# Performance work log

Hardware: AMD Instinct MI355X
Metric: run time of the kernel (lower is better)

Reference implementation:

```python
import jax, jax.numpy as jnp
import numpy as np

DIM = 128
HEADS = 8
DK = DIM // HEADS
HID = DIM * 4
# torch: scores / math.sqrt(scale) with scale = 1/dim**0.5  ->  multiply by dim**0.25
INV = float(1.0 / np.sqrt(1.0 / np.sqrt(DIM)))


def _ln(x, g, b, eps=1e-5):
    m = jnp.mean(x, axis=-1, keepdims=True)
    v = jnp.mean((x - m) ** 2, axis=-1, keepdims=True)
    return (x - m) / jnp.sqrt(v + eps) * g + b


def _lin(x, w, b):  # torch Linear: x @ W.T + b, W:[out,in]
    return jnp.einsum('...i,oi->...o', x, w) + b


def _attention_new(node, edge, w, bv):
    # node [b,n,c], edge [b,n,n,c]; raw torch .view => row-major reshape
    b, n, c = node.shape
    q = _lin(node, w[0], bv[0]).reshape(b, HEADS, n, DK)
    k = _lin(edge, w[1], bv[1]).reshape(b, HEADS, n, n, DK)
    v = _lin(node, w[2], bv[2]).reshape(b, HEADS, n, DK)
    s = jnp.einsum('bhmd,bhmnd->bhmn', q, k) * INV
    out_attn = jax.nn.softmax(s, axis=-1)
    in_attn = jax.nn.softmax(jnp.swapaxes(s, -1, -2), axis=-1)
    eye = jnp.eye(n, dtype=s.dtype)
    # out_attn + in_attn - diag_embed(diagonal(out_attn))
    message = out_attn + in_attn - eye * out_attn
    node_h = jnp.einsum('bhmn,bhnd->bhmd', message, v).reshape(b, n, c)
    edge_h = jnp.einsum('bhmn,bhand->bhamd', message, k).reshape(b, n, n, c)
    return _lin(node_h, w[4], bv[4]), _lin(edge_h, w[3], bv[3]), message


def _enc_dec_attention(mx, px, ma, pa, w, bv):
    b, n, c = mx.shape
    P = px.shape[1]
    qx = _lin(mx, w[0], bv[0]).reshape(b, HEADS, n, DK)
    kx = _lin(px, w[1], bv[1]).reshape(b, HEADS, P, DK)
    vx = _lin(mx, w[2], bv[2]).reshape(b, HEADS, n, DK)
    qa = _lin(ma, w[3], bv[3]).reshape(b, HEADS, n, n, DK)
    ka = _lin(pa, w[4], bv[4]).reshape(b, HEADS, P, P, DK)
    va = _lin(ma, w[5], bv[5]).reshape(b, HEADS, n, n, DK)
    s = jnp.einsum('bhmd,bhnd->bhmn', qx, kx) * INV  # [b,h,n,P]
    out_attn = jax.nn.softmax(s, axis=-1)
    in_attn = jax.nn.softmax(jnp.swapaxes(s, -1, -2), axis=-1)
    message = out_attn + jnp.swapaxes(in_attn, -1, -2)
    # einsum 'bhmn,bhmd->bhmd': sum over n, elementwise scale of v
    node_h = jnp.sum(message, axis=-1)[..., None] * vx
    # 'bhmnd,bhkjd->bhmn': contract d after summing key over (k,j)
    ksum = jnp.sum(ka, axis=(2, 3))  # [b,h,d]
    se = jnp.einsum('bhmnd,bhd->bhmn', qa, ksum) * INV
    oa = jax.nn.softmax(se, axis=-1)
    ia = jax.nn.softmax(jnp.swapaxes(se, -1, -2), axis=-1)
    me = oa + jnp.swapaxes(ia, -1, -2)
    # 'bhmn,bhmkd->bhmnd': contract k
    edge_h = me[..., None] * jnp.sum(va, axis=3)[:, :, :, None, :]
    node_h = _lin(node_h.reshape(b, n, c), w[6], bv[6])
    edge_h = _lin(edge_h.reshape(b, n, n, c), w[7], bv[7])
    return edge_h, node_h, message


def _mlp(x, w1, b1, w2, b2):
    return _lin(jax.nn.sigmoid(_lin(x, w1, b1)), w2, b2)


def _decoder_block(mol_annot, prot_annot, mol_adj, prot_adj,
                   att_w, att_b, dec_w, dec_b,
                   mlp_w1, mlp_b1, mlp_w2, mlp_b2, ln_g, ln_b):
    mx = _ln(mol_annot, ln_g[2], ln_b[2])
    px = _ln(prot_annot, ln_g[3], ln_b[3])
    ma = _ln(mol_adj, ln_g[0], ln_b[0])
    pa = _ln(prot_adj, ln_g[1], ln_b[1])
    px1, pa1, _ = _attention_new(px, pa, att_w, att_b)
    px1 = _ln(px + px1, ln_g[5], ln_b[5])
    pa1 = _ln(pa + pa1, ln_g[4], ln_b[4])
    ma1, mx1, attn_dec = _enc_dec_attention(mx, px1, ma, pa1, dec_w, dec_b)
    ma1 = _ln(ma + ma1, ln_g[6], ln_b[6])
    mx1 = _ln(mx + mx1, ln_g[7], ln_b[7])
    ma2 = _mlp(ma1, mlp_w1[0], mlp_b1[0], mlp_w2[0], mlp_b2[0]) + ma1
    mx2 = _mlp(mx1, mlp_w1[1], mlp_b1[1], mlp_w2[1], mlp_b2[1]) + mx1
    edge_hidden = _ln(ma2, ln_g[8], ln_b[8])
    node_hidden = _ln(mx2, ln_g[9], ln_b[9])
    return edge_hidden, node_hidden, attn_dec


def setup_inputs() -> dict:
    key = jax.random.key(0)
    ks = jax.random.split(key, 16)
    B, N, P = 8, 64, 256
    inp = {
        'mol_annot': jax.random.normal(ks[0], (B, N, DIM), jnp.float32),
        'prot_annot': jax.random.normal(ks[1], (B, P, DIM), jnp.float32),
        'mol_adj': jax.random.normal(ks[2], (B, N, N, DIM), jnp.float32),
        'prot_adj': jax.random.normal(ks[3], (B, P, P, DIM), jnp.float32),
        # Attention_new linears: [q,k,v,out_e,out_n]
        'att_w': jax.random.normal(ks[4], (5, DIM, DIM), jnp.float32) * 0.02,
        'att_b': jax.random.normal(ks[5], (5, DIM), jnp.float32) * 0.02,
        # enc_dec linears: [q_mx,k_px,v_mx,q_ma,k_pa,v_ma,out_mx,out_ma]
        'dec_w': jax.random.normal(ks[6], (8, DIM, DIM), jnp.float32) * 0.02,
        'dec_b': jax.random.normal(ks[7], (8, DIM), jnp.float32) * 0.02,
        # MLPs: index 0 = mlp_ma, 1 = mlp_mx
        'mlp_w1': jax.random.normal(ks[8], (2, HID, DIM), jnp.float32) * 0.02,
        'mlp_b1': jax.random.normal(ks[9], (2, HID), jnp.float32) * 0.02,
        'mlp_w2': jax.random.normal(ks[10], (2, DIM, HID), jnp.float32) * 0.02,
        'mlp_b2': jax.random.normal(ks[11], (2, DIM), jnp.float32) * 0.02,
        # LayerNorms: [ln1_ma,ln1_pa,ln1_mx,ln1_px,ln2_pa,ln2_px,ln3_ma,ln3_mx,ln4_ma,ln4_mx]
        'ln_g': jnp.ones((10, DIM), jnp.float32),
        'ln_b': jnp.zeros((10, DIM), jnp.float32),
    }
    return inp


def reference(mol_annot, prot_annot, mol_adj, prot_adj, att_w, att_b,
              dec_w, dec_b, mlp_w1, mlp_b1, mlp_w2, mlp_b2, ln_g, ln_b):
    return _decoder_block(mol_annot, prot_annot, mol_adj, prot_adj,
                          att_w, att_b, dec_w, dec_b,
                          mlp_w1, mlp_b1, mlp_w2, mlp_b2, ln_g, ln_b)
```

## Files before the change

kernel.cpp:

```cpp
#include <hip/hip_runtime.h>
#include <hip/hip_bf16.h>
#include <math.h>

#define INV_SCALE 3.3635856610148585f

typedef float f32x4 __attribute__((ext_vector_type(4)));
typedef short bf16x8 __attribute__((ext_vector_type(8)));
typedef unsigned short u16;
#define MFMA(a_, b_, c_) __builtin_amdgcn_mfma_f32_16x16x32_bf16(a_, b_, c_, 0, 0, 0)

constexpr int WT_ATT = 0;
constexpr int WT_DEC = 81920;
constexpr int WT_M1  = 212992;
constexpr int WT_M2  = 344064;
constexpr int O_PX   = 475136;
constexpr int O_MX   = 737280;
constexpr int O_MA   = 802816;
constexpr int O_QL   = 4997120;
constexpr int O_VL   = 5259264;
constexpr int O_QXL  = 5521408;
constexpr int O_VXL  = 5586944;
constexpr int O_KXL  = 5652480;
constexpr int O_PX1  = 5914624;
constexpr int O_MX1  = 6176768;
constexpr int O_S    = 6242304;
constexpr int O_MSG  = 10469376;
constexpr int O_NH   = 14663680;
constexpr int O_RS   = 14925824;
constexpr int O_KS   = 14934016;
constexpr int O_SE   = 14935040;
constexpr int O_ME2  = 15197184;
constexpr int O_VAS  = 15459328;
constexpr int O_MROW = 15524864;
constexpr int O_S2   = 15528960;
constexpr int O_MA1  = 16577536;

constexpr int OUT1_OFF = 4194304;
constexpr int OUT2_OFF = 4259840;

__device__ __forceinline__ float waveSum(float v) {
#pragma unroll
  for (int o = 32; o > 0; o >>= 1) v += __shfl_down(v, o, 64);
  return v;
}

__device__ __forceinline__ void split1(float a, u16& h, u16& l) {
  unsigned ua = __float_as_uint(a) & 0xffff0000u;
  h = (u16)(ua >> 16);
  float al = a - __uint_as_float(ua);
  l = (u16)(__float_as_uint(al) >> 16);
}
__device__ __forceinline__ void split8(const float* p, bf16x8& hi, bf16x8& lo) {
#pragma unroll
  for (int i = 0; i < 8; i++) {
    float a = p[i];
    unsigned ua = __float_as_uint(a) & 0xffff0000u;
    float al = a - __uint_as_float(ua);
    hi[i] = (short)(u16)(ua >> 16);
    lo[i] = (short)(u16)(__float_as_uint(al) >> 16);
  }
}
__device__ __forceinline__ u16 rne1(float a) {
  unsigned u = __float_as_uint(a);
  u += 0x7fffu + ((u >> 16) & 1u);
  return (u16)(u >> 16);
}
__device__ __forceinline__ bf16x8 rne8(const float* p) {
  bf16x8 h;
#pragma unroll
  for (int i = 0; i < 8; i++) h[i] = (short)rne1(p[i]);
  return h;
}

__global__ __launch_bounds__(256) void prep_wt(
    const float* __restrict__ att_w, const float* __restrict__ dec_w,
    const float* __restrict__ mlp_w1, const float* __restrict__ mlp_w2,
    float* __restrict__ ws) {
  int seg = blockIdx.x, t = threadIdx.x;
  if (seg < 5) {
    const float* w = att_w + seg * 16384;
    if (seg == 1 || seg == 3) {
      u16* oh = (u16*)(ws + WT_ATT + seg * 16384);
      for (int idx = t; idx < 16384; idx += 256) {
        int e = idx & 7, lane = (idx >> 3) & 63, kk = (idx >> 9) & 3, q = idx >> 11;
        int o = q * 16 + (lane & 15), i = kk * 32 + (lane >> 4) * 8 + e;
        u16 hh, ll; split1(w[o * 128 + i], hh, ll);
        oh[idx] = hh; oh[16384 + idx] = ll;
      }
    } else {
      float* o = ws + WT_ATT + seg * 16384;
      for (int idx = t; idx < 16384; idx += 256) o[idx] = w[(idx & 127) * 128 + (idx >> 7)];
    }
  } else if (seg < 13) {
    int k = seg - 5;
    const float* w = dec_w + k * 16384;
    float* o = ws + WT_DEC + k * 16384;
    for (int idx = t; idx < 16384; idx += 256) o[idx] = w[(idx & 127) * 128 + (idx >> 7)];
  } else if (seg < 15) {
    int k = seg - 13;
    const float* w = mlp_w1 + k * 65536;
    u16* oh = (u16*)(ws + WT_M1 + k * 65536);
    for (int idx = t; idx < 65536; idx += 256) {
      int e = idx & 7, lane = (idx >> 3) & 63, kk = (idx >> 9) & 3, q = idx >> 11;
      int o = q * 16 + (lane & 15), i = kk * 32 + (lane >> 4) * 8 + e;
      oh[idx] = rne1(w[o * 128 + i]); oh[65536 + idx] = 0;
    }
  } else {
    int k = seg - 15;
    const float* w = mlp_w2 + k * 65536;
    u16* oh = (u16*)(ws + WT_M2 + k * 65536);
    for (int idx = t; idx < 65536; idx += 256) {
      int e = idx & 7, lane = (idx >> 3) & 63, kk = (idx >> 9) & 15, q = idx >> 13;
      int o = q * 16 + (lane & 15), i = kk * 32 + (lane >> 4) * 8 + e;
      oh[idx] = rne1(w[o * 512 + i]); oh[65536 + idx] = 0;
    }
  }
}

__global__ __launch_bounds__(128) void ln_rows(const float* __restrict__ in, float* __restrict__ out,
                                               const float* __restrict__ g, const float* __restrict__ b) {
  int row = blockIdx.x, t = threadIdx.x;
  __shared__ float scr[2];
  float x = in[(size_t)row * 128 + t];
  float v = waveSum(x);
  if ((t & 63) == 0) scr[t >> 6] = v;
  __syncthreads();
  float mean = (scr[0] + scr[1]) * (1.f / 128.f);
  __syncthreads();
  float d = x - mean;
  v = waveSum(d * d);
  if ((t & 63) == 0) scr[t >> 6] = v;
  __syncthreads();
  float rstd = rsqrtf((scr[0] + scr[1]) * (1.f / 128.f) + 1e-5f);
  out[(size_t)row * 128 + t] = d * rstd * g[t] + b[t];
}

__global__ __launch_bounds__(128) void lin_rows2(const float* __restrict__ in,
                                                 float* __restrict__ out1, const float* __restrict__ WT1,
                                                 const float* __restrict__ b1v,
                                                 float* __restrict__ out2, const float* __restrict__ WT2,
                                                 const float* __restrict__ b2v) {
  int row = blockIdx.x, t = threadIdx.x;
  __shared__ float rl[128];
  rl[t] = in[(size_t)row * 128 + t];
  __syncthreads();
  float a1 = b1v[t], a2 = b2v[t];
#pragma unroll 8
  for (int i = 0; i < 128; i++) {
    float rv = rl[i];
    a1 += rv * WT1[i * 128 + t];
    a2 += rv * WT2[i * 128 + t];
  }
  out1[(size_t)row * 128 + t] = a1;
  out2[(size_t)row * 128 + t] = a2;
}

__global__ __launch_bounds__(128) void lin_rows(const float* __restrict__ in, float* __restrict__ out,
                                                const float* __restrict__ WT, const float* __restrict__ bias) {
  int row = blockIdx.x, t = threadIdx.x;
  __shared__ float rl[128];
  rl[t] = in[(size_t)row * 128 + t];
  __syncthreads();
  float acc = bias[t];
#pragma unroll 8
  for (int i = 0; i < 128; i++) acc += rl[i] * WT[i * 128 + t];
  out[(size_t)row * 128 + t] = acc;
}

__device__ __forceinline__ void ln32_stats(float (*tile)[132], float* psum, float* meanL, float* rstdL,
                                           int t) {
  int r = t >> 3, seg = t & 7;
  float p = 0;
#pragma unroll
  for (int k = 0; k < 16; k++) p += tile[r][seg * 16 + k];
  psum[r * 8 + seg] = p;
  __syncthreads();
  if (t < 32) { float sm = 0; for (int k = 0; k < 8; k++) sm += psum[t * 8 + k]; meanL[t] = sm * (1.f / 128.f); }
  __syncthreads();
  float mu = meanL[r];
  p = 0;
#pragma unroll
  for (int k = 0; k < 16; k++) { float d = tile[r][seg * 16 + k] - mu; p += d * d; }
  psum[r * 8 + seg] = p;
  __syncthreads();
  if (t < 32) { float sm = 0; for (int k = 0; k < 8; k++) sm += psum[t * 8 + k]; rstdL[t] = rsqrtf(sm * (1.f / 128.f) + 1e-5f); }
  __syncthreads();
}

__device__ __forceinline__ void ln128_stats(float (*tile)[132], float* psum, float* meanL, float* rstdL,
                                            int t) {
  int r = t >> 2, seg = t & 3;
  float p = 0;
#pragma unroll
  for (int k = 0; k < 32; k++) p += tile[r][seg * 32 + k];
  psum[r * 4 + seg] = p;
  __syncthreads();
  if (t < 128) meanL[t] = (psum[t * 4] + psum[t * 4 + 1] + psum[t * 4 + 2] + psum[t * 4 + 3]) * (1.f / 128.f);
  __syncthreads();
  float mu = meanL[r];
  p = 0;
#pragma unroll
  for (int k = 0; k < 32; k++) { float d = tile[r][seg * 32 + k] - mu; p += d * d; }
  psum[r * 4 + seg] = p;
  __syncthreads();
  if (t < 128) rstdL[t] = rsqrtf((psum[t * 4] + psum[t * 4 + 1] + psum[t * 4 + 2] + psum[t * 4 + 3]) * (1.f / 128.f) + 1e-5f);
  __syncthreads();
}

__global__ __launch_bounds__(256, 8) void k1_fold(
    const float* __restrict__ prot_adj, const float* __restrict__ q_lin,
    const float* __restrict__ wk_orig,
    const float* __restrict__ bk,
    const float* __restrict__ g1, const float* __restrict__ b1,
    float* __restrict__ sdst) {
  __shared__ __align__(16) float paF[32][132];
  __shared__ float wq[8][132];
  __shared__ float qL[16];
  __shared__ float psum[256];
  __shared__ float meanL[32], rstdL[32];
  int t = threadIdx.x, bid = blockIdx.x;
  int b = bid >> 11, h = (bid >> 8) & 7, ai = bid & 255;
  int irow = h * 32 + (ai >> 3), j0 = (ai & 7) * 32;
  int mq = (ai >> 3) * 8 + (ai & 7);
  size_t pabase = (((size_t)(b * 256) + irow) * 256 + j0) * 128;
  {
    const float4* src4 = (const float4*)(prot_adj + pabase);
    for (int idx = t; idx < 1024; idx += 256)
      *(float4*)&paF[idx >> 5][(idx & 31) * 4] = src4[idx];
  }
  if (t < 16) qL[t] = q_lin[((size_t)(b * 256) + h * 32 + (mq >> 3)) * 128 + (mq & 7) * 16 + t];
  __syncthreads();
#pragma unroll
  for (int k = 0; k < 4; k++) {
    int o = t + k * 256;
    int g8 = o >> 7, c = o & 127;
    float s = 0;
#pragma unroll
    for (int d = 0; d < 16; d++) s += qL[d] * wk_orig[(g8 * 16 + d) * 128 + c];
    wq[g8][c] = s;
  }
  ln32_stats(paF, psum, meanL, rstdL, t);
  for (int idx = t; idx < 4096; idx += 256) {
    int r = idx >> 7, c = idx & 127;
    paF[r][c] = (paF[r][c] - meanL[r]) * rstdL[r] * g1[c] + b1[c];
  }
  __syncthreads();
  int r = t >> 3, g8 = t & 7;
  float acc = 0;
#pragma unroll
  for (int d = 0; d < 16; d++) acc += qL[d] * bk[g8 * 16 + d];
#pragma unroll 8
  for (int c = 0; c < 128; c++) acc += paF[r][c] * wq[g8][c];
  size_t sb = ((size_t)((b * 8 + h) * 256 + mq)) * 256;
  sdst[sb + t] = INV_SCALE * acc;
}

__global__ __launch_bounds__(256) void col_part(const float* __restrict__ s, float* __restrict__ pmax,
                                                float* __restrict__ psumv) {
  int bid = blockIdx.x, t = threadIdx.x;
  int bh = bid >> 3, ch = bid & 7;
  const float* sp = s + ((size_t)(bh * 256) + ch * 32) * 256 + t;
  float rm = -3.4e38f, rs = 0.f;
  for (int r = 0; r < 32; r++) {
    float x = sp[(size_t)r * 256];
    float nm = fmaxf(rm, x);
    rs = rs * __expf(rm - nm) + __expf(x - nm);
    rm = nm;
  }
  pmax[(bh * 8 + ch) * 256 + t] = rm;
  psumv[(bh * 8 + ch) * 256 + t] = rs;
}

__global__ __launch_bounds__(256, 1) void msg_tiles(const float* __restrict__ s,
                                                    const float* __restrict__ pmax, const float* __restrict__ psumv,
                                                    const float* __restrict__ v_lin,
                                                    u16* __restrict__ mhi, u16* __restrict__ mlo,
                                                    float* __restrict__ nh) {
  __shared__ __align__(16) float rowT[32][260];
  __shared__ float sT[256][33];
  __shared__ __align__(16) u16 vTh[16][264];
  __shared__ __align__(16) u16 vTl[16][264];
  __shared__ float red[256];
  __shared__ float rmax[32], rsinv[32], cmaxL[32], csinvL[32];
  int bid = blockIdx.x, t = threadIdx.x;
  int bh = bid >> 3, m0 = (bid & 7) * 32;
  int b = bh >> 3, h = bh & 7;
  size_t sbase = (size_t)(bh * 256) * 256;
  for (int idx = t; idx < 2048; idx += 256) {
    int r = idx >> 6, c4 = (idx & 63) * 4;
    *(float4*)&rowT[r][c4] = *(const float4*)&s[sbase + (size_t)(m0 + r) * 256 + c4];
  }
  for (int idx = t; idx < 2048; idx += 256) {
    int n = idx >> 3, mc4 = (idx & 7) * 4;
    float4 v4 = *(const float4*)&s[sbase + (size_t)n * 256 + m0 + mc4];
    sT[n][mc4] = v4.x; sT[n][mc4 + 1] = v4.y; sT[n][mc4 + 2] = v4.z; sT[n][mc4 + 3] = v4.w;
  }
  {
    const float4* vb4 = (const float4*)(v_lin + ((size_t)(b * 256) + h * 32) * 128);
    for (int idx = t; idx < 1024; idx += 256) {
      float4 v4 = vb4[idx];
#pragma unroll
      for (int i = 0; i < 4; i++) {
        int flat = idx * 4 + i;
        int d = flat & 15, n = flat >> 4;
        u16 hh2, ll2; split1(((const float*)&v4)[i], hh2, ll2);
        vTh[d][n] = hh2; vTl[d][n] = ll2;
      }
    }
  }
  __syncthreads();
  {
    int r = t >> 3, sg = t & 7;
    float pm = -3.4e38f;
    for (int k = 0; k < 32; k++) pm = fmaxf(pm, rowT[r][sg * 32 + k]);
    red[t] = pm;
    __syncthreads();
    if (t < 32) { float mm = red[t * 8]; for (int k = 1; k < 8; k++) mm = fmaxf(mm, red[t * 8 + k]); rmax[t] = mm; }
    __syncthreads();
    float mm = rmax[r], ps = 0;
    for (int k = 0; k < 32; k++) ps += __expf(rowT[r][sg * 32 + k] - mm);
    red[t] = ps;
    __syncthreads();
    if (t < 32) { float sm = 0; for (int k = 0; k < 8; k++) sm += red[t * 8 + k]; rsinv[t] = 1.f / sm; }
    if (t >= 64 && t < 96) {
      int mc = t - 64, col = m0 + mc;
      float cm = -3.4e38f;
      for (int c2 = 0; c2 < 8; c2++) cm = fmaxf(cm, pmax[(bh * 8 + c2) * 256 + col]);
      float cs = 0;
      for (int c2 = 0; c2 < 8; c2++) cs += psumv[(bh * 8 + c2) * 256 + col] * __expf(pmax[(bh * 8 + c2) * 256 + col] - cm);
      cmaxL[mc] = cm; csinvL[mc] = 1.f / cs;
    }
    __syncthreads();
  }
  for (int idx = t; idx < 8192; idx += 256) {
    int r = idx >> 8, n = idx & 255;
    float x = rowT[r][n];
    float outv = __expf(x - rmax[r]) * rsinv[r];
    float inval = __expf(sT[n][r] - cmaxL[r]) * csinvL[r];
    rowT[r][n] = (n == m0 + r) ? inval : (outv + inval);
  }
  __syncthreads();
  for (int fi = t; fi < 1024; fi += 256) {
    int r = fi >> 5, fc = fi & 31;
    int m = m0 + r;
    int lane = (fc & 3) * 16 + (m & 15);
    size_t base = (size_t)bh * 65536 + (size_t)(m >> 4) * 4096 + (size_t)(fc >> 2) * 512 + lane * 8;
    bf16x8 h8, l8;
    split8(&rowT[r][fc * 8], h8, l8);
    *(bf16x8*)&mhi[base] = h8;
    *(bf16x8*)&mlo[base] = l8;
  }
  int w = t >> 6, l = t & 63, lr = l & 15, lk = l >> 4;
  if (w < 2) {
    f32x4 acc = (f32x4){0.f, 0.f, 0.f, 0.f};
#pragma unroll
    for (int kk = 0; kk < 8; kk++) {
      bf16x8 ah, al;
      split8(&rowT[w * 16 + lr][kk * 32 + lk * 8], ah, al);
      bf16x8 bhv = *(const bf16x8*)&vTh[lr][kk * 32 + lk * 8];
      bf16x8 blv = *(const bf16x8*)&vTl[lr][kk * 32 + lk * 8];
      acc = MFMA(ah, bhv, acc);
      acc = MFMA(al, bhv, acc);
      acc = MFMA(ah, blv, acc);
    }
#pragma unroll
    for (int j = 0; j < 4; j++)
      nh[((size_t)(bh * 256) + m0 + w * 16 + lk * 4 + j) * 16 + lr] = acc[j];
  }
}

__global__ __launch_bounds__(128) void px1_kernel(const float* __restrict__ px, const float* __restrict__ nh,
                                                  const float* __restrict__ WT, const float* __restrict__ bias,
                                                  const float* __restrict__ g, const float* __restrict__ bt,
                                                  float* __restrict__ px1) {
  int p = blockIdx.x, t = threadIdx.x;
  int b = p >> 8, pl = p & 255, h = pl >> 5;
  __shared__ float nodeL[128];
  __shared__ float scr[2];
  nodeL[t] = nh[((size_t)(b * 8 + h) * 256 + ((pl & 31) * 8 + (t >> 4))) * 16 + (t & 15)];
  __syncthreads();
  float acc = bias[t];
#pragma unroll 8
  for (int i = 0; i < 128; i++) acc += nodeL[i] * WT[i * 128 + t];
  float val = px[(size_t)p * 128 + t] + acc;
  float v = waveSum(val);
  if ((t & 63) == 0) scr[t >> 6] = v;
  __syncthreads();
  float mean = (scr[0] + scr[1]) * (1.f / 128.f);
  __syncthreads();
  float dd = val - mean;
  v = waveSum(dd * dd);
  if ((t & 63) == 0) scr[t >> 6] = v;
  __syncthreads();
  float rstd = rsqrtf((scr[0] + scr[1]) * (1.f / 128.f) + 1e-5f);
  px1[(size_t)p * 128 + t] = dd * rstd * g[t] + bt[t];
}

__global__ __launch_bounds__(256, 1) void s2_fused(const float* __restrict__ qxl, const float* __restrict__ kxl,
                                                   float* __restrict__ out2, float* __restrict__ mrow) {
  __shared__ float kxL[256 * 17];
  __shared__ float qxL[64 * 17];
  __shared__ float sL[64][257];
  __shared__ float rmaxL[64], rsinv[64];
  __shared__ float cmaxL[256], csinv[256];
  int bh = blockIdx.x, t = threadIdx.x;
  int b = bh >> 3, h = bh & 7;
  for (int idx = t; idx < 4096; idx += 256) {
    int pl = idx >> 7, cc = idx & 127;
    kxL[(pl * 8 + (cc >> 4)) * 17 + (cc & 15)] = kxl[((size_t)(b * 256) + h * 32 + pl) * 128 + cc];
  }
  for (int idx = t; idx < 1024; idx += 256) {
    int rl = idx >> 7, cc = idx & 127;
    qxL[(rl * 8 + (cc >> 4)) * 17 + (cc & 15)] = qxl[((size_t)(b * 64) + h * 8 + rl) * 128 + cc];
  }
  __syncthreads();
  {
    float kr[16];
#pragma unroll
    for (int d = 0; d < 16; d++) kr[d] = kxL[t * 17 + d];
    for (int m = 0; m < 64; m++) {
      float dot = 0;
#pragma unroll
      for (int d = 0; d < 16; d++) dot += qxL[m * 17 + d] * kr[d];
      sL[m][t] = INV_SCALE * dot;
    }
  }
  __syncthreads();
  if (t < 64) {
    float mx = -3.4e38f;
    for (int p = 0; p < 256; p++) mx = fmaxf(mx, sL[t][p]);
    float sm = 0;
    for (int p = 0; p < 256; p++) sm += __expf(sL[t][p] - mx);
    rmaxL[t] = mx; rsinv[t] = 1.f / sm;
  }
  {
    float mx = -3.4e38f;
    for (int m = 0; m < 64; m++) mx = fmaxf(mx, sL[m][t]);
    float sm = 0;
    for (int m = 0; m < 64; m++) sm += __expf(sL[m][t] - mx);
    cmaxL[t] = mx; csinv[t] = 1.f / sm;
  }
  __syncthreads();
  for (int idx = t; idx < 16384; idx += 256) {
    int m = idx >> 8, p = idx & 255;
    float x = sL[m][p];
    float val = __expf(x - rmaxL[m]) * rsinv[m] + __expf(x - cmaxL[p]) * csinv[p];
    out2[(size_t)bh * 16384 + idx] = val;
    sL[m][p] = val;
  }
  __syncthreads();
  if (t < 64) {
    float sm = 0;
    for (int p = 0; p < 256; p++) sm += sL[t][p];
    mrow[bh * 64 + t] = sm;
  }
}

__global__ __launch_bounds__(128) void mx1_kernel(const float* __restrict__ mx, const float* __restrict__ mrow,
                                                  const float* __restrict__ vxl, const float* __restrict__ WT,
                                                  const float* __restrict__ bias, const float* __restrict__ g,
                                                  const float* __restrict__ bt, float* __restrict__ mx1) {
  int rg = blockIdx.x, t = threadIdx.x;
  int b = rg >> 6, rl = rg & 63, h = rl >> 3;
  __shared__ float nodeL[128];
  __shared__ float scr[2];
  int m = (rl & 7) * 8 + (t >> 4);
  float vxv = vxl[((size_t)(b * 64) + h * 8 + (m >> 3)) * 128 + (m & 7) * 16 + (t & 15)];
  nodeL[t] = mrow[(b * 8 + h) * 64 + m] * vxv;
  __syncthreads();
  float acc = bias[t];
#pragma unroll 8
  for (int i = 0; i < 128; i++) acc += nodeL[i] * WT[i * 128 + t];
  float val = mx[(size_t)rg * 128 + t] + acc;
  float v = waveSum(val);
  if ((t & 63) == 0) scr[t >> 6] = v;
  __syncthreads();
  float mean = (scr[0] + scr[1]) * (1.f / 128.f);
  __syncthreads();
  float dd = val - mean;
  v = waveSum(dd * dd);
  if ((t & 63) == 0) scr[t >> 6] = v;
  __syncthreads();
  float rstd = rsqrtf((scr[0] + scr[1]) * (1.f / 128.f) + 1e-5f);
  mx1[(size_t)rg * 128 + t] = dd * rstd * g[t] + bt[t];
}

__global__ __launch_bounds__(512, 2) void k5_row(
    const float* __restrict__ prot_adj,
    const u16* __restrict__ msg_hi, const u16* __restrict__ msg_lo,
    const u16* __restrict__ wk_hi,
    const u16* __restrict__ wo_hi,
    const float* __restrict__ bk, const float* __restrict__ bo,
    const float* __restrict__ g1, const float* __restrict__ b1,
    const float* __restrict__ g4, const float* __restrict__ b4,
    float* __restrict__ rs128) {
  __shared__ __align__(16) unsigned char Lmem[140800];
  float (*paF)[132] = (float(*)[132])Lmem;
  u16* kBh = (u16*)(Lmem + 67584);
  u16* kBl = (u16*)(Lmem + 67584 + 33792);
  float (*e2)[132] = (float(*)[132])(Lmem + 67584);
  float* psum  = (float*)(Lmem + 135168);
  float* meanL = (float*)(Lmem + 137216);
  float* rstdL = (float*)(Lmem + 137728);
  float* accL  = (float*)(Lmem + 138240);
  float* scr2  = (float*)(Lmem + 138752);
  int t = threadIdx.x;
  int bid = (blockIdx.x & 7) * 256 + (blockIdx.x >> 3);
  int b = bid >> 8, h = (bid >> 5) & 7, irow_rel = bid & 31;
  int irow = h * 32 + irow_rel;
  int w = t >> 6, l = t & 63;
  const int lr = l & 15, lk = l >> 4;
  const size_t mb = ((size_t)(b * 8 + h)) << 16;
  if (t < 128) accL[t] = 0.f;
  for (int half = 0; half < 2; half++) {
    __syncthreads();
    {
      size_t pabase = (((size_t)(b * 256) + irow) * 256 + half * 128) * 128;
      const float4* src4 = (const float4*)(prot_adj + pabase);
      for (int idx = t; idx < 4096; idx += 512)
        *(float4*)&paF[idx >> 5][(idx & 31) * 4] = src4[idx];
    }
    __syncthreads();
    ln128_stats(paF, psum, meanL, rstdL, t);
    for (int idx = t; idx < 16384; idx += 512) {
      int r = idx >> 7, c = idx & 127;
      paF[r][c] = (paF[r][c] - meanL[r]) * rstdL[r] * g1[c] + b1[c];
    }
    __syncthreads();
    for (int pass = 0; pass < 2; pass++) {
      f32x4 acc1[4];
#pragma unroll
      for (int nt = 0; nt < 4; nt++) acc1[nt] = (f32x4){0.f, 0.f, 0.f, 0.f};
#pragma unroll 1
      for (int kk = 0; kk < 4; kk++) {
        bf16x8 ah, al;
        split8(&paF[w * 16 + lr][kk * 32 + lk * 8], ah, al);
#pragma unroll
        for (int nt = 0; nt < 4; nt++) {
          int q = pass * 4 + nt;
          bf16x8 bh = *(const bf16x8*)&wk_hi[q * 2048 + kk * 512 + l * 8];
          bf16x8 bl = *(const bf16x8*)&wk_hi[16384 + q * 2048 + kk * 512 + l * 8];
          acc1[nt] = MFMA(ah, bh, acc1[nt]);
          acc1[nt] = MFMA(al, bh, acc1[nt]);
          acc1[nt] = MFMA(ah, bl, acc1[nt]);
        }
      }
#pragma unroll
      for (int nt = 0; nt < 4; nt++) {
        int q = pass * 4 + nt;
        float bkv = bk[q * 16 + lr];
#pragma unroll
        for (int j = 0; j < 4; j++) {
          int rloc = w * 16 + lk * 4 + j;
          int n = (rloc & 31) * 8 + q;
          int colB = (rloc >> 5) * 16 + lr;
          u16 hh, ll; split1(acc1[nt][j] + bkv, hh, ll);
          kBh[colB * 264 + n] = hh; kBl[colB * 264 + n] = ll;
        }
      }
    }
    __syncthreads();
    f32x4 eacc[2][4];
#pragma unroll
    for (int mt = 0; mt < 2; mt++)
#pragma unroll
      for (int ct = 0; ct < 4; ct++) eacc[mt][ct] = (f32x4){0.f, 0.f, 0.f, 0.f};
#pragma unroll 1
    for (int kk = 0; kk < 8; kk++) {
      bf16x8 bhv[4], blv[4];
#pragma unroll
      for (int ct = 0; ct < 4; ct++) {
        bhv[ct] = *(const bf16x8*)&kBh[(ct * 16 + lr) * 264 + kk * 32 + lk * 8];
        blv[ct] = *(const bf16x8*)&kBl[(ct * 16 + lr) * 264 + kk * 32 + lk * 8];
      }
#pragma unroll
      for (int mt = 0; mt < 2; mt++) {
        size_t ro = mb + (size_t)((w * 2 + mt) * 4096 + kk * 512 + l * 8);
        bf16x8 ah = *(const bf16x8*)&msg_hi[ro];
        bf16x8 al = *(const bf16x8*)&msg_lo[ro];
#pragma unroll
        for (int ct = 0; ct < 4; ct++) {
          eacc[mt][ct] = MFMA(ah, bhv[ct], eacc[mt][ct]);
          eacc[mt][ct] = MFMA(al, bhv[ct], eacc[mt][ct]);
          eacc[mt][ct] = MFMA(ah, blv[ct], eacc[mt][ct]);
        }
      }
    }
    __syncthreads();
#pragma unroll
    for (int mt = 0; mt < 2; mt++)
#pragma unroll
      for (int ct = 0; ct < 4; ct++)
#pragma unroll
        for (int j = 0; j < 4; j++) {
          int m = w * 32 + mt * 16 + lk * 4 + j;
          int colE = ct * 16 + lr;
          e2[(colE >> 4) * 32 + (m >> 3)][(m & 7) * 16 + (colE & 15)] = eacc[mt][ct][j];
        }
    __syncthreads();
    for (int pass = 0; pass < 2; pass++) {
      f32x4 oacc[4];
#pragma unroll
      for (int nt = 0; nt < 4; nt++) oacc[nt] = (f32x4){0.f, 0.f, 0.f, 0.f};
#pragma unroll 1
      for (int kk = 0; kk < 4; kk++) {
        bf16x8 ah, al;
        split8(&e2[w * 16 + lr][kk * 32 + lk * 8], ah, al);
#pragma unroll
        for (int nt = 0; nt < 4; nt++) {
          int q = pass * 4 + nt;
          bf16x8 bh = *(const bf16x8*)&wo_hi[q * 2048 + kk * 512 + l * 8];
          bf16x8 bl = *(const bf16x8*)&wo_hi[16384 + q * 2048 + kk * 512 + l * 8];
          oacc[nt] = MFMA(ah, bh, oacc[nt]);
          oacc[nt] = MFMA(al, bh, oacc[nt]);
          oacc[nt] = MFMA(ah, bl, oacc[nt]);
        }
      }
#pragma unroll
      for (int nt = 0; nt < 4; nt++) {
        int o = (pass * 4 + nt) * 16 + lr;
        float bv = bo[o];
#pragma unroll
        for (int j = 0; j < 4; j++) {
          int rloc = w * 16 + lk * 4 + j;
          paF[rloc][o] = oacc[nt][j] + bv + paF[rloc][o];
        }
      }
    }
    __syncthreads();
    ln128_stats(paF, psum, meanL, rstdL, t);
    {
      int c = t & 127, rh = t >> 7;
      float part = 0;
#pragma unroll
      for (int rr = 0; rr < 32; rr++) {
        int r2 = rh * 32 + rr;
        part += (paF[r2][c] - meanL[r2]) * rstdL[r2];
      }
      scr2[rh * 128 + c] = part;
    }
    __syncthreads();
    if (t < 128) accL[t] += scr2[t] + scr2[128 + t] + scr2[256 + t] + scr2[384 + t];
  }
  __syncthreads();
  if (t < 128)
    atomicAdd(&rs128[(b * 8 + h) * 128 + t], g4[t] * accL[t] + 256.f * b4[t]);
}

__global__ __launch_bounds__(128) void ksum_kernel(const float* __restrict__ rs128, const float* __restrict__ WT,
                                                   const float* __restrict__ bias, float* __restrict__ ks) {
  int bh = blockIdx.x, t = threadIdx.x;
  __shared__ float rsL[128];
  __shared__ float pcL[128];
  rsL[t] = rs128[bh * 128 + t];
  __syncthreads();
  float pc = 0;
#pragma unroll 8
  for (int i = 0; i < 128; i++) pc += rsL[i] * WT[i * 128 + t];
  pcL[t] = pc;
  __syncthreads();
  if (t < 16) {
    float kv = 0;
    for (int g8 = 0; g8 < 8; g8++) kv += pcL[g8 * 16 + t] + 8192.f * bias[g8 * 16 + t];
    ks[bh * 16 + t] = kv;
  }
}

__global__ __launch_bounds__(256) void se_vasum(
    const float* __restrict__ ma, const float* __restrict__ WTqa, const float* __restrict__ bqa,
    const float* __restrict__ WTva, const float* __restrict__ bva,
    const float* __restrict__ ks, float* __restrict__ se, float* __restrict__ vas) {
  __shared__ __align__(16) float w[16384];
  __shared__ float rows[16 * 129];
  __shared__ float red[4096];
  int t = threadIdx.x, bid = blockIdx.x;
  int b = bid >> 8, iq = (bid >> 2) & 63, jb = bid & 3, j0 = jb * 16;
  int h = iq >> 3;
  float ksumv[16];
#pragma unroll
  for (int d = 0; d < 16; d++) ksumv[d] = ks[(b * 8 + h) * 16 + d];
  size_t rowbase = ((size_t)(b * 64 + iq) * 64 + j0) * 128;
  for (int idx = t; idx < 2048; idx += 256) rows[(idx >> 7) * 129 + (idx & 127)] = ma[rowbase + idx];
  for (int idx = t; idx < 16384; idx += 256) w[idx] = WTqa[idx];
  __syncthreads();
  int g8 = t >> 5, r = (t >> 1) & 15, iseg = t & 1;
  {
    float acc[16];
#pragma unroll
    for (int d = 0; d < 16; d++) acc[d] = 0.f;
    for (int ii = 0; ii < 64; ii++) {
      int i2 = iseg * 64 + ii;
      float pav = rows[r * 129 + i2];
      float wv[16];
      const float4* w4 = (const float4*)&w[i2 * 128 + g8 * 16];
      *(float4*)&wv[0] = w4[0]; *(float4*)&wv[4] = w4[1]; *(float4*)&wv[8] = w4[2]; *(float4*)&wv[12] = w4[3];
#pragma unroll
      for (int d = 0; d < 16; d++) acc[d] += pav * wv[d];
    }
    float sval = 0;
#pragma unroll
    for (int d = 0; d < 16; d++) sval += acc[d] * ksumv[d];
    red[(r * 8 + g8) * 2 + iseg] = sval;
    __syncthreads();
    if (t < 128) {
      int rr = t >> 3, gg = t & 7;
      float sv = red[(rr * 8 + gg) * 2] + red[(rr * 8 + gg) * 2 + 1];
      float bdot = 0;
#pragma unroll
      for (int d = 0; d < 16; d++) bdot += bqa[gg * 16 + d] * ksumv[d];
      sv += bdot;
      int jj = j0 + rr;
      int mm = (iq & 7) * 8 + (jj >> 3);
      int n2 = (jj & 7) * 8 + gg;
      se[((size_t)(b * 8 + h) * 64 + mm) * 64 + n2] = INV_SCALE * sv;
    }
    __syncthreads();
  }
  for (int idx = t; idx < 16384; idx += 256) w[idx] = WTva[idx];
  __syncthreads();
  {
    float acc[16];
#pragma unroll
    for (int d = 0; d < 16; d++) acc[d] = 0.f;
    for (int ii = 0; ii < 64; ii++) {
      int i2 = iseg * 64 + ii;
      float pav = rows[r * 129 + i2];
      float wv[16];
      const float4* w4 = (const float4*)&w[i2 * 128 + g8 * 16];
      *(float4*)&wv[0] = w4[0]; *(float4*)&wv[4] = w4[1]; *(float4*)&wv[8] = w4[2]; *(float4*)&wv[12] = w4[3];
#pragma unroll
      for (int d = 0; d < 16; d++) acc[d] += pav * wv[d];
    }
    if (iseg == 0) {
#pragma unroll
      for (int d = 0; d < 16; d++) acc[d] += bva[g8 * 16 + d];
    }
#pragma unroll
    for (int d = 0; d < 16; d++) red[t * 16 + d] = acc[d];
    __syncthreads();
    if (t < 32) {
      int mgrp = t >> 4, d = t & 15;
      float sm = 0;
      for (int gg = 0; gg < 8; gg++)
        for (int rr = mgrp * 8; rr < mgrp * 8 + 8; rr++) {
          sm += red[(gg * 32 + rr * 2) * 16 + d] + red[(gg * 32 + rr * 2 + 1) * 16 + d];
        }
      int mv = (iq & 7) * 8 + jb * 2 + mgrp;
      atomicAdd(&vas[((size_t)(b * 8 + h) * 64 + mv) * 16 + d], sm);
    }
  }
}

__global__ __launch_bounds__(256) void me2_kernel(const float* __restrict__ se, float* __restrict__ me2) {
  __shared__ float sL[64 * 65];
  __shared__ float rmaxL[64], rsinv[64], cmaxL[64], csinv[64];
  int bh = blockIdx.x, t = threadIdx.x;
  for (int idx = t; idx < 4096; idx += 256) sL[(idx >> 6) * 65 + (idx & 63)] = se[(size_t)bh * 4096 + idx];
  __syncthreads();
  if (t < 64) {
    float mx = -3.4e38f;
    for (int n = 0; n < 64; n++) mx = fmaxf(mx, sL[t * 65 + n]);
    float sm = 0;
    for (int n = 0; n < 64; n++) sm += __expf(sL[t * 65 + n] - mx);
    rmaxL[t] = mx; rsinv[t] = 1.f / sm;
  } else if (t < 128) {
    int n = t - 64;
    float mx = -3.4e38f;
    for (int m = 0; m < 64; m++) mx = fmaxf(mx, sL[m * 65 + n]);
    float sm = 0;
    for (int m = 0; m < 64; m++) sm += __expf(sL[m * 65 + n] - mx);
    cmaxL[n] = mx; csinv[n] = 1.f / sm;
  }
  __syncthreads();
  for (int idx = t; idx < 4096; idx += 256) {
    int m = idx >> 6, n = idx & 63;
    float x = sL[m * 65 + n];
    me2[(size_t)bh * 4096 + idx] = __expf(x - rmaxL[m]) * rsinv[m] + __expf(x - cmaxL[n]) * csinv[n];
  }
}

__global__ __launch_bounds__(256) void ma1_kernel(
    const float* __restrict__ ma, const float* __restrict__ me2, const float* __restrict__ vas,
    const float* __restrict__ WT, const float* __restrict__ bias,
    const float* __restrict__ g, const float* __restrict__ bt, float* __restrict__ ma1) {
  __shared__ __align__(16) float w[16384];
  __shared__ float rows[16 * 129];
  __shared__ float ored[4096];
  __shared__ float psum[256];
  __shared__ float meanL[16], rstdL[16];
  int t = threadIdx.x, bid = blockIdx.x;
  int b = bid >> 8, iq = (bid >> 2) & 63, jb = bid & 3, j0 = jb * 16;
  int h = iq >> 3;
  int bh64 = (b * 8 + h) * 64;
  size_t rowbase = ((size_t)(b * 64 + iq) * 64 + j0) * 128;
  for (int idx = t; idx < 2048; idx += 256) {
    int r = idx >> 7, c = idx & 127;
    int mm = (iq & 7) * 8 + jb * 2 + (r >> 3);
    int nn = (r & 7) * 8 + (c >> 4);
    rows[r * 129 + c] = me2[(size_t)(bh64 + mm) * 64 + nn] * vas[(size_t)(bh64 + mm) * 16 + (c & 15)];
  }
  for (int idx = t; idx < 16384; idx += 256) w[idx] = WT[idx];
  __syncthreads();
  int g8 = t >> 5, r = (t >> 1) & 15, iseg = t & 1;
  {
    float acc[16];
#pragma unroll
    for (int d = 0; d < 16; d++) acc[d] = 0.f;
    for (int ii = 0; ii < 64; ii++) {
      int i2 = iseg * 64 + ii;
      float pav = rows[r * 129 + i2];
      float wv[16];
      const float4* w4 = (const float4*)&w[i2 * 128 + g8 * 16];
      *(float4*)&wv[0] = w4[0]; *(float4*)&wv[4] = w4[1]; *(float4*)&wv[8] = w4[2]; *(float4*)&wv[12] = w4[3];
#pragma unroll
      for (int d = 0; d < 16; d++) acc[d] += pav * wv[d];
    }
    float* od = &ored[(iseg * 16 + r) * 128 + g8 * 16];
#pragma unroll
    for (int d = 0; d < 16; d++) od[d] = acc[d];
  }
  __syncthreads();
  for (int idx = t; idx < 2048; idx += 256) {
    int r2 = idx >> 7, c = idx & 127;
    rows[r2 * 129 + c] = ored[r2 * 128 + c] + ored[(16 + r2) * 128 + c] + bias[c] + ma[rowbase + idx];
  }
  __syncthreads();
  {
    int rr = t >> 4, seg = t & 15;
    float p = 0;
#pragma unroll
    for (int k = 0; k < 8; k++) p += rows[rr * 129 + seg * 8 + k];
    psum[rr * 16 + seg] = p;
    __syncthreads();
    if (t < 16) { float sm = 0; for (int k = 0; k < 16; k++) sm += psum[t * 16 + k]; meanL[t] = sm * (1.f / 128.f); }
    __syncthreads();
    float mu = meanL[rr];
    p = 0;
#pragma unroll
    for (int k = 0; k < 8; k++) { float d = rows[rr * 129 + seg * 8 + k] - mu; p += d * d; }
    psum[rr * 16 + seg] = p;
    __syncthreads();
    if (t < 16) { float sm = 0; for (int k = 0; k < 16; k++) sm += psum[t * 16 + k]; rstdL[t] = rsqrtf(sm * (1.f / 128.f) + 1e-5f); }
    __syncthreads();
  }
  for (int idx = t; idx < 2048; idx += 256) {
    int r2 = idx >> 7, c = idx & 127;
    ma1[rowbase + idx] = (rows[r2 * 129 + c] - meanL[r2]) * rstdL[r2] * g[c] + bt[c];
  }
}

__global__ __launch_bounds__(256, 4) void mlp_mfma(
    const float* __restrict__ in,
    const u16* __restrict__ w1h,
    const float* __restrict__ b1,
    const u16* __restrict__ w2h,
    const float* __restrict__ b2,
    const float* __restrict__ g, const float* __restrict__ bt, float* __restrict__ out) {
  __shared__ __align__(16) float rowL[16][132];
  __shared__ __align__(16) u16 hh[16][520];
  __shared__ float psum[256];
  __shared__ float meanL[16], rstdL[16];
  int t = threadIdx.x, bid = blockIdx.x;
  int w = t >> 6, l = t & 63, lr = l & 15, lk = l >> 4;
  size_t base = (size_t)bid * 2048;
  {
    const float4* src4 = (const float4*)(in + base);
    for (int idx = t; idx < 512; idx += 256)
      *(float4*)&rowL[idx >> 5][(idx & 31) * 4] = src4[idx];
  }
  __syncthreads();
  {
    f32x4 acc1[8];
#pragma unroll
    for (int nt = 0; nt < 8; nt++) acc1[nt] = (f32x4){0.f, 0.f, 0.f, 0.f};
#pragma unroll 1
    for (int kk = 0; kk < 4; kk++) {
      bf16x8 ah = rne8(&rowL[lr][kk * 32 + lk * 8]);
#pragma unroll
      for (int nt = 0; nt < 8; nt++) {
        int q = w * 8 + nt;
        bf16x8 bh = *(const bf16x8*)&w1h[q * 2048 + kk * 512 + l * 8];
        acc1[nt] = MFMA(ah, bh, acc1[nt]);
      }
    }
#pragma unroll
    for (int nt = 0; nt < 8; nt++) {
      int o = w * 128 + nt * 16 + lr;
      float bb = b1[o];
#pragma unroll
      for (int j = 0; j < 4; j++) {
        int m = lk * 4 + j;
        float hv = 1.f / (1.f + __expf(-(acc1[nt][j] + bb)));
        hh[m][o] = rne1(hv);
      }
    }
  }
  __syncthreads();
  {
    f32x4 acc2[2];
#pragma unroll
    for (int nt = 0; nt < 2; nt++) acc2[nt] = (f32x4){0.f, 0.f, 0.f, 0.f};
#pragma unroll 1
    for (int kk = 0; kk < 16; kk++) {
      bf16x8 ah = *(const bf16x8*)&hh[lr][kk * 32 + lk * 8];
#pragma unroll
      for (int nt = 0; nt < 2; nt++) {
        int q = w * 2 + nt;
        bf16x8 bh = *(const bf16x8*)&w2h[q * 8192 + kk * 512 + l * 8];
        acc2[nt] = MFMA(ah, bh, acc2[nt]);
      }
    }
    __syncthreads();
#pragma unroll
    for (int nt = 0; nt < 2; nt++) {
      int c = w * 32 + nt * 16 + lr;
      float bb = b2[c];
#pragma unroll
      for (int j = 0; j < 4; j++) {
        int m = lk * 4 + j;
        rowL[m][c] = acc2[nt][j] + bb + rowL[m][c];
      }
    }
  }
  __syncthreads();
  {
    int rr = t >> 4, seg = t & 15;
    float p = 0;
#pragma unroll
    for (int k = 0; k < 8; k++) p += rowL[rr][seg * 8 + k];
    psum[rr * 16 + seg] = p;
    __syncthreads();
    if (t < 16) { float sm = 0; for (int k = 0; k < 16; k++) sm += psum[t * 16 + k]; meanL[t] = sm * (1.f / 128.f); }
    __syncthreads();
    float mu = meanL[rr];
    p = 0;
#pragma unroll
    for (int k = 0; k < 8; k++) { float d = rowL[rr][seg * 8 + k] - mu; p += d * d; }
    psum[rr * 16 + seg] = p;
    __syncthreads();
    if (t < 16) { float sm = 0; for (int k = 0; k < 16; k++) sm += psum[t * 16 + k]; rstdL[t] = rsqrtf(sm * (1.f / 128.f) + 1e-5f); }
    __syncthreads();
  }
  for (int idx = t; idx < 2048; idx += 256) {
    int r2 = idx >> 7, cc = idx & 127;
    out[base + idx] = (rowL[r2][cc] - meanL[r2]) * rstdL[r2] * g[cc] + bt[cc];
  }
}

extern "C" void kernel_launch(void* const* d_in, const int* in_sizes, int n_in,
                              void* d_out, int out_size, void* d_ws, size_t ws_size,
                              hipStream_t stream) {
  (void)in_sizes; (void)n_in; (void)out_size; (void)ws_size;
  const float* mol_annot  = (const float*)d_in[0];
  const float* prot_annot = (const float*)d_in[1];
  const float* mol_adj    = (const float*)d_in[2];
  const float* prot_adj   = (const float*)d_in[3];
  const float* att_w = (const float*)d_in[4];
  const float* att_b = (const float*)d_in[5];
  const float* dec_w = (const float*)d_in[6];
  const float* dec_b = (const float*)d_in[7];
  const float* mlp_w1 = (const float*)d_in[8];
  const float* mlp_b1 = (const float*)d_in[9];
  const float* mlp_w2 = (const float*)d_in[10];
  const float* mlp_b2 = (const float*)d_in[11];
  const float* ln_g = (const float*)d_in[12];
  const float* ln_b = (const float*)d_in[13];
  float* out = (float*)d_out;
  float* ws = (float*)d_ws;

  const u16* wk_hi = (const u16*)(ws + WT_ATT + 16384);
  const u16* wo_hi = (const u16*)(ws + WT_ATT + 3 * 16384);
  u16* msg_hi = (u16*)(ws + O_MA1);
  u16* msg_lo = msg_hi + 4194304;
  float* pmaxp = ws + O_MSG;
  float* psump = ws + O_MSG + 131072;

  hipMemsetAsync(ws + O_RS, 0, 8192 * sizeof(float), stream);
  hipMemsetAsync(ws + O_VAS, 0, 65536 * sizeof(float), stream);
  prep_wt<<<17, 256, 0, stream>>>(att_w, dec_w, mlp_w1, mlp_w2, ws);
  ln_rows<<<2048, 128, 0, stream>>>(prot_annot, ws + O_PX, ln_g + 384, ln_b + 384);
  ln_rows<<<512, 128, 0, stream>>>(mol_annot, ws + O_MX, ln_g + 256, ln_b + 256);
  ln_rows<<<32768, 128, 0, stream>>>(mol_adj, ws + O_MA, ln_g, ln_b);
  lin_rows2<<<2048, 128, 0, stream>>>(ws + O_PX, ws + O_QL, ws + WT_ATT, att_b,
                                      ws + O_VL, ws + WT_ATT + 2 * 16384, att_b + 256);
  lin_rows2<<<512, 128, 0, stream>>>(ws + O_MX, ws + O_QXL, ws + WT_DEC, dec_b,
                                     ws + O_VXL, ws + WT_DEC + 2 * 16384, dec_b + 256);
  k1_fold<<<16384, 256, 0, stream>>>(prot_adj, ws + O_QL, att_w + 16384, att_b + 128,
                                     ln_g + 128, ln_b + 128, ws + O_S);
  col_part<<<512, 256, 0, stream>>>(ws + O_S, pmaxp, psump);
  msg_tiles<<<512, 256, 0, stream>>>(ws + O_S, pmaxp, psump, ws + O_VL, msg_hi, msg_lo, ws + O_NH);
  px1_kernel<<<2048, 128, 0, stream>>>(ws + O_PX, ws + O_NH, ws + WT_ATT + 4 * 16384, att_b + 512,
                                       ln_g + 640, ln_b + 640, ws + O_PX1);
  lin_rows<<<2048, 128, 0, stream>>>(ws + O_PX1, ws + O_KXL, ws + WT_DEC + 16384, dec_b + 128);
  s2_fused<<<64, 256, 0, stream>>>(ws + O_QXL, ws + O_KXL, out + OUT2_OFF, ws + O_MROW);
  mx1_kernel<<<512, 128, 0, stream>>>(ws + O_MX, ws + O_MROW, ws + O_VXL, ws + WT_DEC + 6 * 16384,
                                      dec_b + 768, ln_g + 896, ln_b + 896, ws + O_MX1);
  k5_row<<<2048, 512, 0, stream>>>(prot_adj, msg_hi, msg_lo, wk_hi, wo_hi,
                                   att_b + 128, att_b + 384,
                                   ln_g + 128, ln_b + 128, ln_g + 512, ln_b + 512, ws + O_RS);
  ksum_kernel<<<64, 128, 0, stream>>>(ws + O_RS, ws + WT_DEC + 4 * 16384, dec_b + 512, ws + O_KS);
  se_vasum<<<2048, 256, 0, stream>>>(ws + O_MA, ws + WT_DEC + 3 * 16384, dec_b + 384,
                                     ws + WT_DEC + 5 * 16384, dec_b + 640, ws + O_KS, ws + O_SE, ws + O_VAS);
  me2_kernel<<<64, 256, 0, stream>>>(ws + O_SE, ws + O_ME2);
  ma1_kernel<<<2048, 256, 0, stream>>>(ws + O_MA, ws + O_ME2, ws + O_VAS, ws + WT_DEC + 7 * 16384,
                                       dec_b + 896, ln_g + 768, ln_b + 768, ws + O_MA1);
  mlp_mfma<<<2048, 256, 0, stream>>>(ws + O_MA1, (const u16*)(ws + WT_M1), mlp_b1,
                                     (const u16*)(ws + WT_M2), mlp_b2,
                                     ln_g + 1024, ln_b + 1024, out);
  mlp_mfma<<<32, 256, 0, stream>>>(ws + O_MX1, (const u16*)(ws + WT_M1 + 65536), mlp_b1 + 512,
                                   (const u16*)(ws + WT_M2 + 65536), mlp_b2 + 128,
                                   ln_g + 1152, ln_b + 1152, out + OUT1_OFF);
}
```

Before: 901.2 us.

## Vectorize LayerNorm rows, widen s2_fused to 512 threads, merge k5_row MFMA passes

LayerNorm now handles four rows per 128-thread block with float4 loads and wave shuffles, with no shared-memory barriers. s2_fused runs with 512 threads, splitting the score computation across two halves of query rows. In k5_row the two 4-tile MFMA passes become one 8-tile pass, reusing the split A fragment and adding a barrier before the output writes into paF. This raises register pressure in k5_row, which may lower occupancy.

```diff
diff --git a/kernel.cpp b/kernel.cpp
--- a/kernel.cpp
+++ b/kernel.cpp
@@ -117,22 +117,29 @@
   }
 }
 
-__global__ __launch_bounds__(128) void ln_rows(const float* __restrict__ in, float* __restrict__ out,
-                                               const float* __restrict__ g, const float* __restrict__ b) {
-  int row = blockIdx.x, t = threadIdx.x;
-  __shared__ float scr[2];
-  float x = in[(size_t)row * 128 + t];
-  float v = waveSum(x);
-  if ((t & 63) == 0) scr[t >> 6] = v;
-  __syncthreads();
-  float mean = (scr[0] + scr[1]) * (1.f / 128.f);
-  __syncthreads();
-  float d = x - mean;
-  v = waveSum(d * d);
-  if ((t & 63) == 0) scr[t >> 6] = v;
-  __syncthreads();
-  float rstd = rsqrtf((scr[0] + scr[1]) * (1.f / 128.f) + 1e-5f);
-  out[(size_t)row * 128 + t] = d * rstd * g[t] + b[t];
+__global__ __launch_bounds__(128) void ln_rows4(const float* __restrict__ in, float* __restrict__ out,
+                                                const float* __restrict__ g, const float* __restrict__ b) {
+  int t = threadIdx.x;
+  size_t row = (size_t)blockIdx.x * 4 + (t >> 5);
+  int c4 = (t & 31) * 4;
+  float4 x = *(const float4*)&in[row * 128 + c4];
+  float s = x.x + x.y + x.z + x.w;
+#pragma unroll
+  for (int o = 16; o > 0; o >>= 1) s += __shfl_xor(s, o, 64);
+  float mean = s * (1.f / 128.f);
+  float dx = x.x - mean, dy = x.y - mean, dz = x.z - mean, dw = x.w - mean;
+  float v = dx * dx + dy * dy + dz * dz + dw * dw;
+#pragma unroll
+  for (int o = 16; o > 0; o >>= 1) v += __shfl_xor(v, o, 64);
+  float rstd = rsqrtf(v * (1.f / 128.f) + 1e-5f);
+  float4 gv = *(const float4*)&g[c4];
+  float4 bv = *(const float4*)&b[c4];
+  float4 o4;
+  o4.x = dx * rstd * gv.x + bv.x;
+  o4.y = dy * rstd * gv.y + bv.y;
+  o4.z = dz * rstd * gv.z + bv.z;
+  o4.w = dw * rstd * gv.w + bv.w;
+  *(float4*)&out[row * 128 + c4] = o4;
 }
 
 __global__ __launch_bounds__(128) void lin_rows2(const float* __restrict__ in,
@@ -396,7 +403,7 @@
   px1[(size_t)p * 128 + t] = dd * rstd * g[t] + bt[t];
 }
 
-__global__ __launch_bounds__(256, 1) void s2_fused(const float* __restrict__ qxl, const float* __restrict__ kxl,
+__global__ __launch_bounds__(512, 1) void s2_fused(const float* __restrict__ qxl, const float* __restrict__ kxl,
                                                    float* __restrict__ out2, float* __restrict__ mrow) {
   __shared__ float kxL[256 * 17];
   __shared__ float qxL[64 * 17];
@@ -405,24 +412,25 @@
   __shared__ float cmaxL[256], csinv[256];
   int bh = blockIdx.x, t = threadIdx.x;
   int b = bh >> 3, h = bh & 7;
-  for (int idx = t; idx < 4096; idx += 256) {
+  for (int idx = t; idx < 4096; idx += 512) {
     int pl = idx >> 7, cc = idx & 127;
     kxL[(pl * 8 + (cc >> 4)) * 17 + (cc & 15)] = kxl[((size_t)(b * 256) + h * 32 + pl) * 128 + cc];
   }
-  for (int idx = t; idx < 1024; idx += 256) {
+  for (int idx = t; idx < 1024; idx += 512) {
     int rl = idx >> 7, cc = idx & 127;
     qxL[(rl * 8 + (cc >> 4)) * 17 + (cc & 15)] = qxl[((size_t)(b * 64) + h * 8 + rl) * 128 + cc];
   }
   __syncthreads();
   {
+    int p = t & 255, mh = t >> 8;
     float kr[16];
 #pragma unroll
-    for (int d = 0; d < 16; d++) kr[d] = kxL[t * 17 + d];
-    for (int m = 0; m < 64; m++) {
+    for (int d = 0; d < 16; d++) kr[d] = kxL[p * 17 + d];
+    for (int m = mh * 32; m < mh * 32 + 32; m++) {
       float dot = 0;
 #pragma unroll
       for (int d = 0; d < 16; d++) dot += qxL[m * 17 + d] * kr[d];
-      sL[m][t] = INV_SCALE * dot;
+      sL[m][p] = INV_SCALE * dot;
     }
   }
   __syncthreads();
@@ -433,7 +441,7 @@
     for (int p = 0; p < 256; p++) sm += __expf(sL[t][p] - mx);
     rmaxL[t] = mx; rsinv[t] = 1.f / sm;
   }
-  {
+  if (t < 256) {
     float mx = -3.4e38f;
     for (int m = 0; m < 64; m++) mx = fmaxf(mx, sL[m][t]);
     float sm = 0;
@@ -441,7 +449,7 @@
     cmaxL[t] = mx; csinv[t] = 1.f / sm;
   }
   __syncthreads();
-  for (int idx = t; idx < 16384; idx += 256) {
+  for (int idx = t; idx < 16384; idx += 512) {
     int m = idx >> 8, p = idx & 255;
     float x = sL[m][p];
     float val = __expf(x - rmaxL[m]) * rsinv[m] + __expf(x - cmaxL[p]) * csinv[p];
@@ -527,34 +535,32 @@
       paF[r][c] = (paF[r][c] - meanL[r]) * rstdL[r] * g1[c] + b1[c];
     }
     __syncthreads();
-    for (int pass = 0; pass < 2; pass++) {
-      f32x4 acc1[4];
-#pragma unroll
-      for (int nt = 0; nt < 4; nt++) acc1[nt] = (f32x4){0.f, 0.f, 0.f, 0.f};
+    {
+      f32x4 acc1[8];
+#pragma unroll
+      for (int q = 0; q < 8; q++) acc1[q] = (f32x4){0.f, 0.f, 0.f, 0.f};
 #pragma unroll 1
       for (int kk = 0; kk < 4; kk++) {
         bf16x8 ah, al;
         split8(&paF[w * 16 + lr][kk * 32 + lk * 8], ah, al);
 #pragma unroll
-        for (int nt = 0; nt < 4; nt++) {
-          int q = pass * 4 + nt;
+        for (int q = 0; q < 8; q++) {
           bf16x8 bh = *(const bf16x8*)&wk_hi[q * 2048 + kk * 512 + l * 8];
           bf16x8 bl = *(const bf16x8*)&wk_hi[16384 + q * 2048 + kk * 512 + l * 8];
-          acc1[nt] = MFMA(ah, bh, acc1[nt]);
-          acc1[nt] = MFMA(al, bh, acc1[nt]);
-          acc1[nt] = MFMA(ah, bl, acc1[nt]);
+          acc1[q] = MFMA(ah, bh, acc1[q]);
+          acc1[q] = MFMA(al, bh, acc1[q]);
+          acc1[q] = MFMA(ah, bl, acc1[q]);
         }
       }
 #pragma unroll
-      for (int nt = 0; nt < 4; nt++) {
-        int q = pass * 4 + nt;
+      for (int q = 0; q < 8; q++) {
         float bkv = bk[q * 16 + lr];
 #pragma unroll
         for (int j = 0; j < 4; j++) {
           int rloc = w * 16 + lk * 4 + j;
           int n = (rloc & 31) * 8 + q;
           int colB = (rloc >> 5) * 16 + lr;
-          u16 hh, ll; split1(acc1[nt][j] + bkv, hh, ll);
+          u16 hh, ll; split1(acc1[q][j] + bkv, hh, ll);
           kBh[colB * 264 + n] = hh; kBl[colB * 264 + n] = ll;
         }
       }
@@ -598,32 +604,32 @@
           e2[(colE >> 4) * 32 + (m >> 3)][(m & 7) * 16 + (colE & 15)] = eacc[mt][ct][j];
         }
     __syncthreads();
-    for (int pass = 0; pass < 2; pass++) {
-      f32x4 oacc[4];
-#pragma unroll
-      for (int nt = 0; nt < 4; nt++) oacc[nt] = (f32x4){0.f, 0.f, 0.f, 0.f};
+    {
+      f32x4 oacc[8];
+#pragma unroll
+      for (int q = 0; q < 8; q++) oacc[q] = (f32x4){0.f, 0.f, 0.f, 0.f};
 #pragma unroll 1
       for (int kk = 0; kk < 4; kk++) {
         bf16x8 ah, al;
         split8(&e2[w * 16 + lr][kk * 32 + lk * 8], ah, al);
 #pragma unroll
-        for (int nt = 0; nt < 4; nt++) {
-          int q = pass * 4 + nt;
+        for (int q = 0; q < 8; q++) {
           bf16x8 bh = *(const bf16x8*)&wo_hi[q * 2048 + kk * 512 + l * 8];
           bf16x8 bl = *(const bf16x8*)&wo_hi[16384 + q * 2048 + kk * 512 + l * 8];
-          oacc[nt] = MFMA(ah, bh, oacc[nt]);
-          oacc[nt] = MFMA(al, bh, oacc[nt]);
-          oacc[nt] = MFMA(ah, bl, oacc[nt]);
+          oacc[q] = MFMA(ah, bh, oacc[q]);
+          oacc[q] = MFMA(al, bh, oacc[q]);
+          oacc[q] = MFMA(ah, bl, oacc[q]);
         }
       }
-#pragma unroll
-      for (int nt = 0; nt < 4; nt++) {
-        int o = (pass * 4 + nt) * 16 + lr;
+      __syncthreads();
+#pragma unroll
+      for (int q = 0; q < 8; q++) {
+        int o = q * 16 + lr;
         float bv = bo[o];
 #pragma unroll
         for (int j = 0; j < 4; j++) {
           int rloc = w * 16 + lk * 4 + j;
-          paF[rloc][o] = oacc[nt][j] + bv + paF[rloc][o];
+          paF[rloc][o] = oacc[q][j] + bv + paF[rloc][o];
         }
       }
     }
@@ -978,9 +984,9 @@
   hipMemsetAsync(ws + O_RS, 0, 8192 * sizeof(float), stream);
   hipMemsetAsync(ws + O_VAS, 0, 65536 * sizeof(float), stream);
   prep_wt<<<17, 256, 0, stream>>>(att_w, dec_w, mlp_w1, mlp_w2, ws);
-  ln_rows<<<2048, 128, 0, stream>>>(prot_annot, ws + O_PX, ln_g + 384, ln_b + 384);
-  ln_rows<<<512, 128, 0, stream>>>(mol_annot, ws + O_MX, ln_g + 256, ln_b + 256);
-  ln_rows<<<32768, 128, 0, stream>>>(mol_adj, ws + O_MA, ln_g, ln_b);
+  ln_rows4<<<512, 128, 0, stream>>>(prot_annot, ws + O_PX, ln_g + 384, ln_b + 384);
+  ln_rows4<<<128, 128, 0, stream>>>(mol_annot, ws + O_MX, ln_g + 256, ln_b + 256);
+  ln_rows4<<<8192, 128, 0, stream>>>(mol_adj, ws + O_MA, ln_g, ln_b);
   lin_rows2<<<2048, 128, 0, stream>>>(ws + O_PX, ws + O_QL, ws + WT_ATT, att_b,
                                       ws + O_VL, ws + WT_ATT + 2 * 16384, att_b + 256);
   lin_rows2<<<512, 128, 0, stream>>>(ws + O_MX, ws + O_QXL, ws + WT_DEC, dec_b,
@@ -992,7 +998,7 @@
   px1_kernel<<<2048, 128, 0, stream>>>(ws + O_PX, ws + O_NH, ws + WT_ATT + 4 * 16384, att_b + 512,
                                        ln_g + 640, ln_b + 640, ws + O_PX1);
   lin_rows<<<2048, 128, 0, stream>>>(ws + O_PX1, ws + O_KXL, ws + WT_DEC + 16384, dec_b + 128);
-  s2_fused<<<64, 256, 0, stream>>>(ws + O_QXL, ws + O_KXL, out + OUT2_OFF, ws + O_MROW);
+  s2_fused<<<64, 512, 0, stream>>>(ws + O_QXL, ws + O_KXL, out + OUT2_OFF, ws + O_MROW);
   mx1_kernel<<<512, 128, 0, stream>>>(ws + O_MX, ws + O_MROW, ws + O_VXL, ws + WT_DEC + 6 * 16384,
                                       dec_b + 768, ln_g + 896, ln_b + 896, ws + O_MX1);
   k5_row<<<2048, 512, 0, stream>>>(prot_adj, msg_hi, msg_lo, wk_hi, wo_hi,
```

Result: no change. 891.4 us (-1.1%).
